# Kernel optimization log

Measured on AMD Instinct MI355X. Metric: run time of the kernel, lower is better.

Reference implementation:

```python
import jax, jax.numpy as jnp
import numpy as np

BLOCKS = (1, 2, 3, 4)      # (block_size, offset=0) from max_block_size=4
BLOCK_MULT = 12            # lcm(1,2,3,4)
DS = 4                     # downsample_factor
MAX_BS = 4                 # max block size (also pos_conv kernel size)
DIM = 512
VOCAB = 256


def _masked_mean(t, m, axis):
    # t: [..., L, D], m: [..., L] bool -> mean over axis with mask, 0 where empty
    mf = m[..., None].astype(t.dtype)
    num = jnp.sum(t * mf, axis=axis)
    tot = jnp.sum(mf, axis=axis)
    mean = num / jnp.clip(tot, 1.0)
    return jnp.where(tot == 0.0, jnp.zeros_like(mean), mean)


def setup_inputs() -> dict:
    key = jax.random.key(0)
    ks = jax.random.split(key, 8)
    B, S = 8, 2048
    return {
        "x": jax.random.randint(ks[0], (B, S), 0, VOCAB),
        "mask": jnp.ones((B, S), dtype=bool),
        "emb": jax.random.normal(ks[1], (VOCAB, DIM), jnp.float32) * 0.02,
        "dw_w": jax.random.normal(ks[2], (MAX_BS, 1, DIM), jnp.float32) * 0.1,   # depthwise kernel (W, I=1, O=DIM)
        "dw_b": jnp.zeros((DIM,), jnp.float32),
        "pw_w": jax.random.normal(ks[3], (1, DIM, DIM), jnp.float32) * 0.03,     # pointwise 1x1 conv
        "pw_b": jnp.zeros((DIM,), jnp.float32),
        "score_w": jax.random.normal(ks[4], (DIM, 1), jnp.float32) * 0.05,
        "score_b": jnp.zeros((1,), jnp.float32),
    }


def reference(x, mask, emb, dw_w, dw_b, pw_w, pw_b, score_w, score_b):
    B, S = x.shape
    D = DIM
    trunc = ((S + DS - 1) // DS) * DS  # next_divisible_length(S, DS); equals S here

    h = emb[x]                                              # [B,S,D]
    h = jnp.pad(h, ((0, 0), (0, MAX_BS - 1), (0, 0)))       # right pad for VALID conv
    dn = jax.lax.conv_dimension_numbers(h.shape, dw_w.shape, ('NWC', 'WIO', 'NWC'))
    h = jax.lax.conv_general_dilated(h, dw_w, (1,), 'VALID',
                                     dimension_numbers=dn,
                                     feature_group_count=D) + dw_b  # depthwise -> [B,S,D]
    h = jnp.einsum('bsd,de->bse', h, pw_w[0]) + pw_b                # pointwise

    # pad seq to multiple of lcm of block sizes
    Sp = ((h.shape[1] + BLOCK_MULT - 1) // BLOCK_MULT) * BLOCK_MULT
    pad = Sp - h.shape[1]
    h = jnp.pad(h, ((0, 0), (0, pad), (0, 0)))
    m = jnp.pad(mask.astype(bool), ((0, 0), (0, pad)), constant_values=False)

    reprs, rmasks = [], []
    for bsz in BLOCKS:  # fixed small set of block sizes (offset=0 for all)
        nb = Sp // bsz
        g = h.reshape(B, nb, bsz, D)
        mg = m.reshape(B, nb, bsz)
        r = _masked_mean(g, mg, axis=2)                       # [B,nb,D]
        reprs.append(jnp.repeat(r, bsz, axis=1))              # [B,Sp,D]
        rmasks.append(jnp.repeat(jnp.any(mg, axis=-1), bsz, axis=1))

    block_reprs = jnp.stack(reprs, axis=2)    # [B,Sp,M,D]
    block_masks = jnp.stack(rmasks, axis=2)   # [B,Sp,M]

    scores = (block_reprs @ score_w)[..., 0] + score_b[0]     # [B,Sp,M]
    max_neg = -jnp.finfo(scores.dtype).max
    scores = jnp.where(block_masks, scores, max_neg)
    scores = jnp.nan_to_num(jax.nn.softmax(scores, axis=2), nan=0.0)

    # consensus attention over positions
    sim = jnp.einsum('bim,bjm->bij', scores, scores)          # [B,Sp,Sp]
    cm = m[:, :, None] & m[:, None, :]
    sim = jnp.where(cm, sim, max_neg)
    attn = jnp.nan_to_num(jax.nn.softmax(sim, axis=-1), nan=0.0)
    scores = jnp.einsum('bij,bjm->bim', attn, scores)

    out = jnp.einsum('bsmd,bsm->bsd', block_reprs, scores)    # weighted combine
    out = out[:, :trunc]
    mt = m[:, :trunc]

    nl = trunc // DS
    xb = out.reshape(B, nl, DS, D)
    mb = mt.reshape(B, nl, DS)
    out = _masked_mean(xb, mb, axis=2)                        # [B, S/DS, D]
    out_mask = jnp.any(mb, axis=-1)
    return out, out_mask
```

## Files before the change

### kernel.cpp

```cpp
#include <hip/hip_runtime.h>
#include <stdint.h>
#include <stddef.h>

typedef __bf16 bf16_t;
typedef bf16_t bf16x4v __attribute__((ext_vector_type(4)));
typedef bf16_t bf16x8v __attribute__((ext_vector_type(8)));
typedef float  f32x4   __attribute__((ext_vector_type(4)));

#define NBATCH 8
#define SEQ    2048
#define DIM    512
#define SP     2052
#define NB2    1026
#define NB3    684
#define NB4    513
#define NL     512
#define NJC    8
#define JCH    257

static __device__ __forceinline__ f32x4 ldbf4(const bf16_t* p) {
  bf16x4v v = *(const bf16x4v*)p;
  f32x4 r;
  r.x = (float)v[0]; r.y = (float)v[1]; r.z = (float)v[2]; r.w = (float)v[3];
  return r;
}
static __device__ __forceinline__ void stbf4(bf16_t* p, f32x4 v) {
  bf16x4v o;
  o[0] = (bf16_t)v.x; o[1] = (bf16_t)v.y; o[2] = (bf16_t)v.z; o[3] = (bf16_t)v.w;
  *(bf16x4v*)p = o;
}

static __device__ __forceinline__ void gload_lds16(const void* g, void* l) {
  __builtin_amdgcn_global_load_lds(
      (const __attribute__((address_space(1))) void*)g,
      (__attribute__((address_space(3))) void*)l, 16, 0, 0);
}

#define GA_WT   1024
#define GA_MASK 65
#define GA_A    (NBATCH * SEQ / 2)
__global__ __launch_bounds__(256) void kA_prep(
    const float* __restrict__ pw, bf16_t* __restrict__ Wt,
    const void* __restrict__ mraw, float* __restrict__ mask01,
    const int* __restrict__ x, const float* __restrict__ emb,
    const float* __restrict__ dww, const float* __restrict__ dwb,
    bf16_t* __restrict__ A) {
  const int bx = blockIdx.x, t = threadIdx.x;
  if (bx < GA_WT) {
    int idx = bx * 256 + t;
    int n = idx >> 9, k = idx & 511;
    Wt[(size_t)n * DIM + k] = (bf16_t)pw[(size_t)k * DIM + n];
    return;
  }
  if (bx < GA_WT + GA_MASK) {
    int idx = (bx - GA_WT) * 256 + t;
    if (idx >= NBATCH * SP) return;
    int b = idx / SP, s = idx - b * SP;
    const unsigned char* mb = (const unsigned char*)mraw;
    int u8 = 0;
#pragma unroll
    for (int i = 0; i < 64; i++)
      if ((i & 3) != 0 && mb[i] != 0) u8 = 1;
    float v = 0.f;
    if (s < SEQ) {
      int mi = b * SEQ + s;
      int nz = u8 ? (mb[mi] != 0) : (((const int*)mraw)[mi] != 0);
      v = nz ? 1.f : 0.f;
    }
    mask01[idx] = v;
    return;
  }
  int rp = bx - (GA_WT + GA_MASK);
  int row = rp * 2 + (t >> 7);
  int b = row >> 11, s = row & 2047;
  int d0 = (t & 127) * 4;
  f32x4 acc = *(const f32x4*)(dwb + d0);
#pragma unroll
  for (int tt = 0; tt < 4; tt++) {
    int sp = s + tt;
    if (sp < SEQ) {
      int v = x[b * SEQ + sp];
      f32x4 e = *(const f32x4*)(emb + (size_t)v * DIM + d0);
      f32x4 w = *(const f32x4*)(dww + tt * DIM + d0);
      acc += e * w;
    }
  }
  stbf4(A + (size_t)row * DIM + d0, acc);
}

#define BM 128
#define BN 128
#define BK 32
__global__ __launch_bounds__(256) void k2_gemm(
    const bf16_t* __restrict__ A, const bf16_t* __restrict__ Bt,
    const float* __restrict__ bias, bf16_t* __restrict__ H) {
  __shared__ __align__(16) bf16_t As[BM * BK];
  __shared__ __align__(16) bf16_t Bs[BN * BK];
  const int t = threadIdx.x;
  const int bid = blockIdx.x;
  const int xcd = bid & 7, loc = bid >> 3;
  const int mt = xcd * 16 + (loc >> 2);
  const int nt = loc & 3;
  const int m0 = mt * BM, n0 = nt * BN;
  const int lane = t & 63, wave = t >> 6;
  const int wm = (wave >> 1) * 64, wn = (wave & 1) * 64;
  const int mloc = lane & 15, quad = lane >> 4;

  f32x4 acc[4][4] = {};

  const int i1 = t, i2 = t + 256;
  char* asd1 = (char*)As + i1 * 16;
  char* asd2 = (char*)As + i2 * 16;
  char* bsd1 = (char*)Bs + i1 * 16;
  char* bsd2 = (char*)Bs + i2 * 16;
  const int ar1 = i1 >> 2, ak1 = (i1 & 3) * 8;
  const int ar2 = i2 >> 2, ak2 = (i2 & 3) * 8;

  for (int k0 = 0; k0 < 512; k0 += BK) {
    gload_lds16(A + (size_t)(m0 + ar1) * DIM + k0 + ak1, asd1);
    gload_lds16(A + (size_t)(m0 + ar2) * DIM + k0 + ak2, asd2);
    gload_lds16(Bt + (size_t)(n0 + ar1) * DIM + k0 + ak1, bsd1);
    gload_lds16(Bt + (size_t)(n0 + ar2) * DIM + k0 + ak2, bsd2);
    __syncthreads();
    bf16x8v af[4], bfr[4];
#pragma unroll
    for (int i = 0; i < 4; i++)
      af[i] = *(const bf16x8v*)&As[(wm + i * 16 + mloc) * BK + quad * 8];
#pragma unroll
    for (int i = 0; i < 4; i++)
      bfr[i] = *(const bf16x8v*)&Bs[(wn + i * 16 + mloc) * BK + quad * 8];
#pragma unroll
    for (int mi = 0; mi < 4; mi++)
#pragma unroll
      for (int ni = 0; ni < 4; ni++)
        acc[mi][ni] = __builtin_amdgcn_mfma_f32_16x16x32_bf16(
            af[mi], bfr[ni], acc[mi][ni], 0, 0, 0);
    __syncthreads();
  }
#pragma unroll
  for (int ni = 0; ni < 4; ni++) {
    int col = n0 + wn + ni * 16 + mloc;
    float bv = bias[col];
#pragma unroll
    for (int mi = 0; mi < 4; mi++) {
      int rbase = m0 + wm + mi * 16 + quad * 4;
#pragma unroll
      for (int r = 0; r < 4; r++)
        H[(size_t)(rbase + r) * DIM + col] = (bf16_t)(acc[mi][ni][r] + bv);
    }
  }
}

__global__ __launch_bounds__(128) void kB_levels(
    const bf16_t* __restrict__ H, const float* __restrict__ mask01,
    const float* __restrict__ sw, const float* __restrict__ sbp,
    bf16_t* __restrict__ R2, bf16_t* __restrict__ R3, bf16_t* __restrict__ R4,
    float* __restrict__ P) {
  const int b = blockIdx.x, c = blockIdx.y;
  const int s0 = c * 12;
  const int t = threadIdx.x;
  const int d0 = t * 4;
  const float sb = sbp[0];

  f32x4 h[12];
  float ms[12], p[12];
  f32x4 swv = *(const f32x4*)(sw + d0);
#pragma unroll
  for (int i = 0; i < 12; i++) {
    int s = s0 + i;
    ms[i] = mask01[b * SP + s];
    if (s < SEQ) {
      h[i] = ldbf4(H + ((size_t)b * SEQ + s) * DIM + d0);
    } else {
      h[i].x = h[i].y = h[i].z = h[i].w = 0.f;
    }
    p[i] = h[i].x * swv.x + h[i].y * swv.y + h[i].z * swv.z + h[i].w * swv.w;
  }
#pragma unroll
  for (int j = 0; j < 6; j++) {
    int i0 = 2 * j;
    float cc = ms[i0] + ms[i0 + 1];
    f32x4 sm = h[i0] * ms[i0] + h[i0 + 1] * ms[i0 + 1];
    float sc = cc > 0.f ? 1.f / cc : 0.f;
    stbf4(R2 + ((size_t)b * NB2 + (c * 6 + j)) * DIM + d0, sm * sc);
  }
#pragma unroll
  for (int j = 0; j < 4; j++) {
    int i0 = 3 * j;
    float cc = ms[i0] + ms[i0 + 1] + ms[i0 + 2];
    f32x4 sm = h[i0] * ms[i0] + h[i0 + 1] * ms[i0 + 1] + h[i0 + 2] * ms[i0 + 2];
    float sc = cc > 0.f ? 1.f / cc : 0.f;
    stbf4(R3 + ((size_t)b * NB3 + (c * 4 + j)) * DIM + d0, sm * sc);
  }
#pragma unroll
  for (int j = 0; j < 3; j++) {
    int i0 = 4 * j;
    float cc = ms[i0] + ms[i0 + 1] + ms[i0 + 2] + ms[i0 + 3];
    f32x4 sm = h[i0] * ms[i0] + h[i0 + 1] * ms[i0 + 1] +
               h[i0 + 2] * ms[i0 + 2] + h[i0 + 3] * ms[i0 + 3];
    float sc = cc > 0.f ? 1.f / cc : 0.f;
    stbf4(R4 + ((size_t)b * NB4 + (c * 3 + j)) * DIM + d0, sm * sc);
  }
#pragma unroll
  for (int off = 32; off > 0; off >>= 1)
#pragma unroll
    for (int i = 0; i < 12; i++) p[i] += __shfl_down(p[i], off);
  __shared__ float hsw[2][12];
  int lane = t & 63, wv = t >> 6;
  if (lane == 0)
#pragma unroll
    for (int i = 0; i < 12; i++) hsw[wv][i] = p[i];
  __syncthreads();
#define HSUM(i) (hsw[0][i] + hsw[1][i])
  if (t < 12) {
    int i = t;
    float m1 = ms[i];
    float v1 = HSUM(i) * m1 + sb;
    int i2 = i & ~1;
    float cc2 = ms[i2] + ms[i2 + 1];
    float s2 = HSUM(i2) * ms[i2] + HSUM(i2 + 1) * ms[i2 + 1];
    float v2 = (cc2 > 0.f ? s2 / cc2 : 0.f) + sb;
    int i3 = (i >= 9) ? 9 : (i >= 6) ? 6 : (i >= 3) ? 3 : 0;
    float cc3 = ms[i3] + ms[i3 + 1] + ms[i3 + 2];
    float s3 = HSUM(i3) * ms[i3] + HSUM(i3 + 1) * ms[i3 + 1] +
               HSUM(i3 + 2) * ms[i3 + 2];
    float v3 = (cc3 > 0.f ? s3 / cc3 : 0.f) + sb;
    int i4 = i & ~3;
    float cc4 = ms[i4] + ms[i4 + 1] + ms[i4 + 2] + ms[i4 + 3];
    float s4 = HSUM(i4) * ms[i4] + HSUM(i4 + 1) * ms[i4 + 1] +
               HSUM(i4 + 2) * ms[i4 + 2] + HSUM(i4 + 3) * ms[i4 + 3];
    float v4 = (cc4 > 0.f ? s4 / cc4 : 0.f) + sb;
    const float NEG = -3.0e38f;
    float a1 = m1 > 0.f ? v1 : NEG, a2 = cc2 > 0.f ? v2 : NEG;
    float a3 = cc3 > 0.f ? v3 : NEG, a4 = cc4 > 0.f ? v4 : NEG;
    float mx = fmaxf(fmaxf(a1, a2), fmaxf(a3, a4));
    f32x4 o;
    if (mx <= NEG) {
      o.x = o.y = o.z = o.w = 0.25f;
    } else {
      float e1 = m1 > 0.f ? __expf(v1 - mx) : 0.f;
      float e2 = cc2 > 0.f ? __expf(v2 - mx) : 0.f;
      float e3 = cc3 > 0.f ? __expf(v3 - mx) : 0.f;
      float e4 = cc4 > 0.f ? __expf(v4 - mx) : 0.f;
      float inv = 1.f / (e1 + e2 + e3 + e4);
      o.x = e1 * inv; o.y = e2 * inv; o.z = e3 * inv; o.w = e4 * inv;
    }
    *(f32x4*)(P + ((size_t)b * SP + s0 + i) * 4) = o;
  }
#undef HSUM
}

__global__ __launch_bounds__(128) void k5_attn(
    const float* __restrict__ P, const float* __restrict__ mask01,
    float* __restrict__ Wacc) {
  const int b = blockIdx.x, it = blockIdx.y, jc = blockIdx.z;
  const int t = threadIdx.x;
  __shared__ f32x4 Q[JCH];
  __shared__ float c2w[2];
  const int j0 = jc * JCH;
  const int len = (j0 + JCH <= SP) ? JCH : (SP - j0);
  float cnt0 = 0.f;
  for (int j = t; j < len; j += 128) {
    f32x4 q = *(const f32x4*)(P + ((size_t)b * SP + j0 + j) * 4);
    float mf = mask01[b * SP + j0 + j];
    if (mf == 0.f) {
      q.x = q.y = q.z = q.w = 0.f;
      cnt0 += 1.f;
    }
    Q[j] = q;
  }
#pragma unroll
  for (int off = 32; off > 0; off >>= 1) cnt0 += __shfl_down(cnt0, off);
  if ((t & 63) == 0) c2w[t >> 6] = cnt0;
  __syncthreads();
  const float nmask = c2w[0] + c2w[1];
  const int i = it * 128 + t;
  f32x4 qi = *(const f32x4*)(P + ((size_t)b * SP + i) * 4);
  float den = -nmask;
  f32x4 acc; acc.x = acc.y = acc.z = acc.w = 0.f;
  for (int j = 0; j < len; j++) {
    f32x4 pj = Q[j];
    float sim = qi.x * pj.x + qi.y * pj.y + qi.z * pj.z + qi.w * pj.w;
    float e = __expf(sim);
    den += e;
    acc += e * pj;
  }
  float* wp = Wacc + (((size_t)jc * NBATCH + b) * SEQ + i) * 5;
  wp[0] = acc.x; wp[1] = acc.y; wp[2] = acc.z; wp[3] = acc.w; wp[4] = den;
}

__global__ __launch_bounds__(128) void k6_out(
    const bf16_t* __restrict__ H, const bf16_t* __restrict__ R2,
    const bf16_t* __restrict__ R3, const bf16_t* __restrict__ R4,
    const float* __restrict__ mask01, const float* __restrict__ Wacc,
    float* __restrict__ out, float* __restrict__ omask) {
  const int b = blockIdx.x, l = blockIdx.y;
  const int t = threadIdx.x;
  const int d0 = t * 4;
  __shared__ f32x4 wsh[4];
  __shared__ float msh[4];
  if (t < 32) {
    int si = t >> 3, jc = t & 7;
    int s = l * 4 + si;
    const float* wp = Wacc + (((size_t)jc * NBATCH + b) * SEQ + s) * 5;
    float n0 = wp[0], n1 = wp[1], n2 = wp[2], n3 = wp[3], dn = wp[4];
#pragma unroll
    for (int off = 4; off > 0; off >>= 1) {
      n0 += __shfl_down(n0, off); n1 += __shfl_down(n1, off);
      n2 += __shfl_down(n2, off); n3 += __shfl_down(n3, off);
      dn += __shfl_down(dn, off);
    }
    if ((t & 7) == 0) {
      float inv = dn > 0.f ? 1.f / dn : 0.f;
      f32x4 w; w.x = n0 * inv; w.y = n1 * inv; w.z = n2 * inv; w.w = n3 * inv;
      wsh[si] = w;
      msh[si] = mask01[b * SP + s];
    }
  }
  __syncthreads();
  f32x4 o; o.x = o.y = o.z = o.w = 0.f;
  float cnt = 0.f;
#pragma unroll
  for (int si = 0; si < 4; si++) {
    int s = l * 4 + si;
    float m = msh[si];
    f32x4 w = wsh[si];
    f32x4 r1 = ldbf4(H + ((size_t)b * SEQ + s) * DIM + d0);
    f32x4 r2 = ldbf4(R2 + ((size_t)b * NB2 + (s >> 1)) * DIM + d0);
    f32x4 r3 = ldbf4(R3 + ((size_t)b * NB3 + (s / 3)) * DIM + d0);
    f32x4 r4 = ldbf4(R4 + ((size_t)b * NB4 + (s >> 2)) * DIM + d0);
    o += m * (w.x * r1 + w.y * r2 + w.z * r3 + w.w * r4);
    cnt += m;
  }
  float inv = cnt > 0.f ? 1.f / cnt : 0.f;
  o *= inv;
  *(f32x4*)(out + ((size_t)b * NL + l) * DIM + d0) = o;
  if (t == 0) omask[b * NL + l] = cnt > 0.f ? 1.f : 0.f;
}

extern "C" void kernel_launch(void* const* d_in, const int* in_sizes, int n_in,
                              void* d_out, int out_size, void* d_ws, size_t ws_size,
                              hipStream_t stream) {
  const int*   x    = (const int*)d_in[0];
  const void*  mraw = d_in[1];
  const float* emb  = (const float*)d_in[2];
  const float* dww  = (const float*)d_in[3];
  const float* dwb  = (const float*)d_in[4];
  const float* pw   = (const float*)d_in[5];
  const float* pwb  = (const float*)d_in[6];
  const float* sw   = (const float*)d_in[7];
  const float* sb   = (const float*)d_in[8];

  char* ws = (char*)d_ws;
  size_t off = 0;
  auto alloc = [&](size_t bytes) {
    size_t o = off;
    off = (off + bytes + 255) & ~(size_t)255;
    return o;
  };
  bf16_t* A    = (bf16_t*)(ws + alloc((size_t)NBATCH * SEQ * DIM * 2));
  bf16_t* H    = (bf16_t*)(ws + alloc((size_t)NBATCH * SEQ * DIM * 2));
  bf16_t* Wt   = (bf16_t*)(ws + alloc((size_t)DIM * DIM * 2));
  bf16_t* R2   = (bf16_t*)(ws + alloc((size_t)NBATCH * NB2 * DIM * 2));
  bf16_t* R3   = (bf16_t*)(ws + alloc((size_t)NBATCH * NB3 * DIM * 2));
  bf16_t* R4   = (bf16_t*)(ws + alloc((size_t)NBATCH * NB4 * DIM * 2));
  float* mask01 = (float*)(ws + alloc((size_t)NBATCH * SP * 4));
  float* P     = (float*)(ws + alloc((size_t)NBATCH * SP * 4 * 4));
  float* Wacc  = (float*)(ws + alloc((size_t)NJC * NBATCH * SEQ * 5 * 4));

  float* out   = (float*)d_out;
  float* omask = out + (size_t)NBATCH * NL * DIM;

  kA_prep<<<GA_WT + GA_MASK + GA_A, 256, 0, stream>>>(pw, Wt, mraw, mask01,
                                                      x, emb, dww, dwb, A);
  k2_gemm<<<512, 256, 0, stream>>>(A, Wt, pwb, H);
  kB_levels<<<dim3(NBATCH, 171), 128, 0, stream>>>(H, mask01, sw, sb,
                                                   R2, R3, R4, P);
  k5_attn<<<dim3(NBATCH, 16, NJC), 128, 0, stream>>>(P, mask01, Wacc);
  k6_out<<<dim3(NBATCH, NL), 128, 0, stream>>>(H, R2, R3, R4, mask01, Wacc,
                                               out, omask);
}
```

Measured before the change: 142.9 us.

## Tile weight transpose through LDS and halve GEMM M-tile for more blocks

The weight transpose in the prep kernel now stages 32x32 tiles in shared memory, so both the reads and the bf16 writes are coalesced and vectorised instead of strided per element. The pointwise GEMM tile shrinks from 128x128 to 64x128 and the grid doubles to 1024 blocks, with the wave layout and XCD mapping adjusted to match. The aim is better occupancy and CU coverage for this 16384x512x512 GEMM, at the cost of reloading the B tile more often and doing less MFMA work per LDS load.

```diff
diff --git a/kernel.cpp b/kernel.cpp
--- a/kernel.cpp
+++ b/kernel.cpp
@@ -36,7 +36,7 @@
       (__attribute__((address_space(3))) void*)l, 16, 0, 0);
 }
 
-#define GA_WT   1024
+#define GA_WT   256
 #define GA_MASK 65
 #define GA_A    (NBATCH * SEQ / 2)
 __global__ __launch_bounds__(256) void kA_prep(
@@ -47,9 +47,17 @@
     bf16_t* __restrict__ A) {
   const int bx = blockIdx.x, t = threadIdx.x;
   if (bx < GA_WT) {
-    int idx = bx * 256 + t;
-    int n = idx >> 9, k = idx & 511;
-    Wt[(size_t)n * DIM + k] = (bf16_t)pw[(size_t)k * DIM + n];
+    __shared__ float T[32][33];
+    int ti = bx >> 4, tj = bx & 15;
+    int r = t >> 3, c0 = (t & 7) * 4;
+    f32x4 v = *(const f32x4*)(pw + (size_t)(ti * 32 + r) * DIM + tj * 32 + c0);
+    T[c0 + 0][r] = v.x; T[c0 + 1][r] = v.y;
+    T[c0 + 2][r] = v.z; T[c0 + 3][r] = v.w;
+    __syncthreads();
+    bf16x4v o;
+    o[0] = (bf16_t)T[r][c0 + 0]; o[1] = (bf16_t)T[r][c0 + 1];
+    o[2] = (bf16_t)T[r][c0 + 2]; o[3] = (bf16_t)T[r][c0 + 3];
+    *(bf16x4v*)(Wt + (size_t)(tj * 32 + r) * DIM + ti * 32 + c0) = o;
     return;
   }
   if (bx < GA_WT + GA_MASK) {
@@ -88,7 +96,7 @@
   stbf4(A + (size_t)row * DIM + d0, acc);
 }
 
-#define BM 128
+#define BM 64
 #define BN 128
 #define BK 32
 __global__ __launch_bounds__(256) void k2_gemm(
@@ -99,38 +107,36 @@
   const int t = threadIdx.x;
   const int bid = blockIdx.x;
   const int xcd = bid & 7, loc = bid >> 3;
-  const int mt = xcd * 16 + (loc >> 2);
+  const int mt = xcd * 32 + (loc >> 2);
   const int nt = loc & 3;
   const int m0 = mt * BM, n0 = nt * BN;
   const int lane = t & 63, wave = t >> 6;
-  const int wm = (wave >> 1) * 64, wn = (wave & 1) * 64;
+  const int wm = (wave & 1) * 32, wn = (wave >> 1) * 64;
   const int mloc = lane & 15, quad = lane >> 4;
 
-  f32x4 acc[4][4] = {};
-
-  const int i1 = t, i2 = t + 256;
-  char* asd1 = (char*)As + i1 * 16;
-  char* asd2 = (char*)As + i2 * 16;
-  char* bsd1 = (char*)Bs + i1 * 16;
-  char* bsd2 = (char*)Bs + i2 * 16;
-  const int ar1 = i1 >> 2, ak1 = (i1 & 3) * 8;
-  const int ar2 = i2 >> 2, ak2 = (i2 & 3) * 8;
+  f32x4 acc[2][4] = {};
+
+  char* asd  = (char*)As + t * 16;
+  char* bsd1 = (char*)Bs + t * 16;
+  char* bsd2 = (char*)Bs + (t + 256) * 16;
+  const int ar = t >> 2,           ak = (t & 3) * 8;
+  const int br1 = t >> 2,          bk1 = (t & 3) * 8;
+  const int br2 = (t + 256) >> 2,  bk2 = (t & 3) * 8;
 
   for (int k0 = 0; k0 < 512; k0 += BK) {
-    gload_lds16(A + (size_t)(m0 + ar1) * DIM + k0 + ak1, asd1);
-    gload_lds16(A + (size_t)(m0 + ar2) * DIM + k0 + ak2, asd2);
-    gload_lds16(Bt + (size_t)(n0 + ar1) * DIM + k0 + ak1, bsd1);
-    gload_lds16(Bt + (size_t)(n0 + ar2) * DIM + k0 + ak2, bsd2);
+    gload_lds16(A + (size_t)(m0 + ar) * DIM + k0 + ak, asd);
+    gload_lds16(Bt + (size_t)(n0 + br1) * DIM + k0 + bk1, bsd1);
+    gload_lds16(Bt + (size_t)(n0 + br2) * DIM + k0 + bk2, bsd2);
     __syncthreads();
-    bf16x8v af[4], bfr[4];
-#pragma unroll
-    for (int i = 0; i < 4; i++)
+    bf16x8v af[2], bfr[4];
+#pragma unroll
+    for (int i = 0; i < 2; i++)
       af[i] = *(const bf16x8v*)&As[(wm + i * 16 + mloc) * BK + quad * 8];
 #pragma unroll
     for (int i = 0; i < 4; i++)
       bfr[i] = *(const bf16x8v*)&Bs[(wn + i * 16 + mloc) * BK + quad * 8];
 #pragma unroll
-    for (int mi = 0; mi < 4; mi++)
+    for (int mi = 0; mi < 2; mi++)
 #pragma unroll
       for (int ni = 0; ni < 4; ni++)
         acc[mi][ni] = __builtin_amdgcn_mfma_f32_16x16x32_bf16(
@@ -142,7 +148,7 @@
     int col = n0 + wn + ni * 16 + mloc;
     float bv = bias[col];
 #pragma unroll
-    for (int mi = 0; mi < 4; mi++) {
+    for (int mi = 0; mi < 2; mi++) {
       int rbase = m0 + wm + mi * 16 + quad * 4;
 #pragma unroll
       for (int r = 0; r < 4; r++)
@@ -373,7 +379,7 @@
 
   kA_prep<<<GA_WT + GA_MASK + GA_A, 256, 0, stream>>>(pw, Wt, mraw, mask01,
                                                       x, emb, dww, dwb, A);
-  k2_gemm<<<512, 256, 0, stream>>>(A, Wt, pwb, H);
+  k2_gemm<<<1024, 256, 0, stream>>>(A, Wt, pwb, H);
   kB_levels<<<dim3(NBATCH, 171), 128, 0, stream>>>(H, mask01, sw, sb,
                                                    R2, R3, R4, P);
   k5_attn<<<dim3(NBATCH, 16, NJC), 128, 0, stream>>>(P, mask01, Wacc);
```

Result: no change. 141.5 us (-1.0%).
